# Performance work log

Measured on AMD Instinct MI355X. Metric: run time of the kernel, lower is better.

The kernel has to match this reference:

```python
import jax, jax.numpy as jnp
import numpy as np

B, L, E = 8, 2048, 128


def setup_inputs() -> dict:
    key = jax.random.key(0)
    k1, k2, k3, k4 = jax.random.split(key, 4)
    return {
        "Uq": jax.random.normal(k1, (B, L, E), dtype=jnp.float32),
        "Uid": jax.random.normal(k2, (B, L, E), dtype=jnp.float32),
        "mask": jnp.ones((L, L), dtype=jnp.float32),
        "Wc_w": jax.random.normal(k3, (3 * E,), dtype=jnp.float32) * 0.05,
        "Wc_b": jax.random.normal(k4, (), dtype=jnp.float32) * 0.05,
    }


def reference(Uq, Uid, mask, Wc_w, Wc_b):
    # Wc(cat(Uid, Uq, Uid*Uq)) decomposed into three direct projections —
    # exact same math as the Linear over the concatenation, never
    # materializing the [B, L, L, 3E] tensor.
    e = Uq.shape[-1]
    w_id, w_q, w_mul = Wc_w[:e], Wc_w[e:2 * e], Wc_w[2 * e:]
    s_id = jnp.einsum("bie,e->bi", Uid, w_id)          # [B, Lid]
    s_q = jnp.einsum("bje,e->bj", Uq, w_q)             # [B, Lq]
    s_mul = jnp.einsum("bie,bje,e->bij", Uid, Uq, w_mul)  # [B, Lid, Lq]
    S = (s_id[:, :, None] + s_q[:, None, :] + s_mul + Wc_b) * mask
    # S_D2Q = Softmax(dim=0) over the per-example [Lid, Lq] matrix -> axis=1
    P = jax.nn.softmax(S, axis=1)                      # [B, Lid, Lq]
    A_D2Q = jnp.einsum("bij,bje->bie", P, Uq)          # [B, Lid, E]
    M = jnp.einsum("bij,bkj->bik", P, P)               # P @ P^T, [B, Lid, Lid]
    A_Q2D = jnp.einsum("bik,bke->bie", M, Uid)         # [B, Lid, E]
    Vid = jnp.concatenate([Uid, A_D2Q, Uid * A_D2Q, Uid * A_Q2D], axis=-1)
    return Vid  # [B, Lid, 4E]
```

## Files before the change

### kernel.cpp

```cpp
#include <hip/hip_runtime.h>

#define L 2048
#define E 128
#define NB 8

typedef float f32x4 __attribute__((ext_vector_type(4)));
typedef short short8 __attribute__((ext_vector_type(8)));
typedef unsigned int u32;

static __device__ inline float bf2f(ushort u) {
  union { float f; u32 i; } v; v.i = ((u32)u) << 16; return v.f;
}
static __device__ inline ushort f2bf(float f) {
  union { float f; u32 i; } v; v.f = f;
  u32 x = v.i;
  return (ushort)((x + 0x7fffu + ((x >> 16) & 1u)) >> 16);
}

__device__ inline void glds16(const ushort* g, ushort* l) {
  __builtin_amdgcn_global_load_lds(
      (const __attribute__((address_space(1))) u32*)(const void*)g,
      (__attribute__((address_space(3))) u32*)(void*)l, 16, 0, 0);
}

__global__ __launch_bounds__(128) void k_prep(const float* __restrict__ Uq,
                                              const float* __restrict__ Uid,
                                              const float* __restrict__ Wcw,
                                              ushort* __restrict__ UqB,
                                              ushort* __restrict__ UidB,
                                              ushort* __restrict__ Uidw,
                                              float* __restrict__ s_id,
                                              float* __restrict__ s_q) {
  int r = blockIdx.x;
  int e = threadIdx.x;
  ushort uqu  = f2bf(Uq[(long)r * E + e]);
  ushort uidu = f2bf(Uid[(long)r * E + e]);
  float uqf = bf2f(uqu), uidf = bf2f(uidu);
  float wid  = bf2f(f2bf(Wcw[e]));
  float wq   = bf2f(f2bf(Wcw[E + e]));
  float wmul = bf2f(f2bf(Wcw[2 * E + e]));
  UqB[(long)r * E + e]  = uqu;
  UidB[(long)r * E + e] = uidu;
  Uidw[(long)r * E + e] = f2bf(uidf * wmul);
  float sid = uidf * wid, sq = uqf * wq;
  #pragma unroll
  for (int off = 32; off >= 1; off >>= 1) {
    sid += __shfl_down(sid, off, 64);
    sq  += __shfl_down(sq,  off, 64);
  }
  __shared__ float red[4];
  int wv = threadIdx.x >> 6;
  if ((threadIdx.x & 63) == 0) { red[wv * 2] = sid; red[wv * 2 + 1] = sq; }
  __syncthreads();
  if (threadIdx.x == 0) { s_id[r] = red[0] + red[2]; s_q[r] = red[1] + red[3]; }
}

__global__ __launch_bounds__(256) void k_maskT(const float* __restrict__ mask,
                                               ushort* __restrict__ maskT) {
  __shared__ ushort tile[32][33];
  int j0 = blockIdx.x * 32, i0 = blockIdx.y * 32;
  int tx = threadIdx.x, ty = threadIdx.y;
  #pragma unroll
  for (int r = ty; r < 32; r += 8)
    tile[r][tx] = f2bf(mask[(long)(i0 + r) * L + j0 + tx]);
  __syncthreads();
  #pragma unroll
  for (int r = ty; r < 32; r += 8)
    maskT[(long)(j0 + r) * L + i0 + tx] = tile[tx][r];
}

__global__ __launch_bounds__(256) void k_tr(const ushort* __restrict__ src,
                                            ushort* __restrict__ dst,
                                            int R, int C) {
  __shared__ ushort tile[32][33];
  long base = (long)blockIdx.z * R * C;
  src += base; dst += base;
  int c0 = blockIdx.x * 32, r0 = blockIdx.y * 32;
  int tx = threadIdx.x, ty = threadIdx.y;
  #pragma unroll
  for (int i = ty; i < 32; i += 8)
    tile[i][tx] = src[(long)(r0 + i) * C + c0 + tx];
  __syncthreads();
  #pragma unroll
  for (int i = ty; i < 32; i += 8)
    dst[(long)(c0 + i) * R + r0 + tx] = tile[tx][i];
}

__device__ inline void gemm128_loop(const ushort* __restrict__ A,
                                    const ushort* __restrict__ B,
                                    long ldA, long ldB, int K,
                                    f32x4 acc[4][4],
                                    ushort* ldsA, ushort* ldsB) {
  const int t = threadIdx.x;
  const int w = t >> 6, lane = t & 63;
  const int mrow = lane & 15, quad = lane >> 4;
  const int lr = lane >> 3;
  const int lc = ((lane & 7) ^ lr) * 8;
  const int mh = (w & 1) * 64, nh = (w >> 1) * 64;
  #pragma unroll
  for (int s = 0; s < 4; s++) {
    int row = w * 32 + s * 8 + lr;
    glds16(&A[(long)row * ldA + lc], &ldsA[w * 2048 + s * 512]);
    glds16(&B[(long)row * ldB + lc], &ldsB[w * 2048 + s * 512]);
  }
  __syncthreads();
  int cur = 0;
  for (int k0 = 0; k0 < K; k0 += 64) {
    int nxt = cur ^ 1;
    if (k0 + 64 < K) {
      #pragma unroll
      for (int s = 0; s < 4; s++) {
        int row = w * 32 + s * 8 + lr;
        glds16(&A[(long)row * ldA + k0 + 64 + lc], &ldsA[nxt * 8192 + w * 2048 + s * 512]);
        glds16(&B[(long)row * ldB + k0 + 64 + lc], &ldsB[nxt * 8192 + w * 2048 + s * 512]);
      }
    }
    const ushort* cA = &ldsA[cur * 8192];
    const ushort* cB = &ldsB[cur * 8192];
    #pragma unroll
    for (int kk = 0; kk < 2; kk++) {
      short8 av[4], bv[4];
      #pragma unroll
      for (int mi = 0; mi < 4; mi++)
        av[mi] = *(const short8*)&cA[(mh + mi * 16 + mrow) * 64 +
                                     ((kk * 32 + quad * 8) ^ ((mrow & 7) << 3))];
      #pragma unroll
      for (int ni = 0; ni < 4; ni++)
        bv[ni] = *(const short8*)&cB[(nh + ni * 16 + mrow) * 64 +
                                     ((kk * 32 + quad * 8) ^ ((mrow & 7) << 3))];
      #pragma unroll
      for (int mi = 0; mi < 4; mi++)
        #pragma unroll
        for (int ni = 0; ni < 4; ni++)
          acc[mi][ni] = __builtin_amdgcn_mfma_f32_16x16x32_bf16(av[mi], bv[ni], acc[mi][ni], 0, 0, 0);
    }
    __syncthreads();
    cur = nxt;
  }
}

__device__ inline void gemm64x128_loop(const ushort* __restrict__ A,
                                       const ushort* __restrict__ B,
                                       long ldA, long ldB, int K,
                                       f32x4 acc[2][4],
                                       ushort* ldsA, ushort* ldsB) {
  const int t = threadIdx.x;
  const int w = t >> 6, lane = t & 63;
  const int mrow = lane & 15, quad = lane >> 4;
  const int lr = lane >> 3;
  const int lc = ((lane & 7) ^ lr) * 8;
  const int mh = (w & 1) * 32, nh = (w >> 1) * 64;
  #pragma unroll
  for (int s = 0; s < 2; s++) {
    int row = w * 16 + s * 8 + lr;
    glds16(&A[(long)row * ldA + lc], &ldsA[w * 1024 + s * 512]);
  }
  #pragma unroll
  for (int s = 0; s < 4; s++) {
    int row = w * 32 + s * 8 + lr;
    glds16(&B[(long)row * ldB + lc], &ldsB[w * 2048 + s * 512]);
  }
  __syncthreads();
  int cur = 0;
  for (int k0 = 0; k0 < K; k0 += 64) {
    int nxt = cur ^ 1;
    if (k0 + 64 < K) {
      #pragma unroll
      for (int s = 0; s < 2; s++) {
        int row = w * 16 + s * 8 + lr;
        glds16(&A[(long)row * ldA + k0 + 64 + lc], &ldsA[nxt * 4096 + w * 1024 + s * 512]);
      }
      #pragma unroll
      for (int s = 0; s < 4; s++) {
        int row = w * 32 + s * 8 + lr;
        glds16(&B[(long)row * ldB + k0 + 64 + lc], &ldsB[nxt * 8192 + w * 2048 + s * 512]);
      }
    }
    const ushort* cA = &ldsA[cur * 4096];
    const ushort* cB = &ldsB[cur * 8192];
    #pragma unroll
    for (int kk = 0; kk < 2; kk++) {
      short8 av[2], bv[4];
      #pragma unroll
      for (int mi = 0; mi < 2; mi++)
        av[mi] = *(const short8*)&cA[(mh + mi * 16 + mrow) * 64 +
                                     ((kk * 32 + quad * 8) ^ ((mrow & 7) << 3))];
      #pragma unroll
      for (int ni = 0; ni < 4; ni++)
        bv[ni] = *(const short8*)&cB[(nh + ni * 16 + mrow) * 64 +
                                     ((kk * 32 + quad * 8) ^ ((mrow & 7) << 3))];
      #pragma unroll
      for (int mi = 0; mi < 2; mi++)
        #pragma unroll
        for (int ni = 0; ni < 4; ni++)
          acc[mi][ni] = __builtin_amdgcn_mfma_f32_16x16x32_bf16(av[mi], bv[ni], acc[mi][ni], 0, 0, 0);
    }
    __syncthreads();
    cur = nxt;
  }
}

__global__ __launch_bounds__(256) void k_scores(const ushort* __restrict__ Uq,
                                                const ushort* __restrict__ Uidw,
                                                const float* __restrict__ s_id,
                                                const float* __restrict__ s_q,
                                                const float* __restrict__ Wcb,
                                                const ushort* __restrict__ maskT,
                                                ushort* __restrict__ St,
                                                float* __restrict__ pm,
                                                float* __restrict__ ps, int b0) {
  __shared__ ushort lds[32768];
  ushort* ldsA = lds;
  ushort* ldsB = lds + 16384;
  int bz = blockIdx.z, b = b0 + bz;
  int m0 = blockIdx.x * 128;
  int n0 = blockIdx.y * 128;
  int tile_i = blockIdx.y;
  const ushort* A = Uq   + (long)b * L * E + (long)m0 * E;
  const ushort* B = Uidw + (long)b * L * E + (long)n0 * E;
  f32x4 acc[4][4] = {};
  gemm128_loop(A, B, E, E, E, acc, ldsA, ldsB);
  float bias = bf2f(f2bf(Wcb[0]));
  const int t = threadIdx.x, w = t >> 6, lane = t & 63;
  const int col = lane & 15, quad = lane >> 4;
  const int mh = (w & 1) * 64, nh = (w >> 1) * 64;

  __syncthreads();
  float sidv[4];
  #pragma unroll
  for (int ni = 0; ni < 4; ni++)
    sidv[ni] = s_id[b * L + n0 + nh + ni * 16 + col];
  #pragma unroll
  for (int mi = 0; mi < 4; mi++) {
    float sqv[4];
    #pragma unroll
    for (int rg = 0; rg < 4; rg++)
      sqv[rg] = s_q[b * L + m0 + mh + mi * 16 + quad * 4 + rg];
    #pragma unroll
    for (int ni = 0; ni < 4; ni++) {
      int cl = nh + ni * 16 + col;
      #pragma unroll
      for (int rg = 0; rg < 4; rg++) {
        int row = mh + mi * 16 + quad * 4 + rg;
        float v = acc[mi][ni][rg] + sqv[rg] + sidv[ni] + bias;
        lds[row * 128 + (cl ^ ((row & 7) << 3))] = f2bf(v);
      }
    }
  }
  __syncthreads();
  #pragma unroll
  for (int p = 0; p < 8; p++) {
    int r2 = p * 16 + (t >> 4);
    int cu = (t & 15) * 8;
    uint4 sv = *(const uint4*)&lds[r2 * 128 + (cu ^ ((r2 & 7) << 3))];
    int jg = m0 + r2;
    uint4 mv = *(const uint4*)&maskT[(long)jg * L + n0 + cu];
    ushort o[8]; float vv[8];
    const ushort* sp = (const ushort*)&sv;
    const ushort* mp = (const ushort*)&mv;
    #pragma unroll
    for (int k = 0; k < 8; k++) {
      o[k] = f2bf(bf2f(sp[k]) * bf2f(mp[k]));
      vv[k] = bf2f(o[k]);
    }
    *(uint4*)&St[(long)bz * L * L + (long)jg * L + n0 + cu] = *(const uint4*)&o[0];
    float lmx = vv[0];
    #pragma unroll
    for (int k = 1; k < 8; k++) lmx = fmaxf(lmx, vv[k]);
    #pragma unroll
    for (int off = 8; off >= 1; off >>= 1) lmx = fmaxf(lmx, __shfl_xor(lmx, off, 64));
    float lsum = 0.f;
    #pragma unroll
    for (int k = 0; k < 8; k++) lsum += __expf(vv[k] - lmx);
    #pragma unroll
    for (int off = 8; off >= 1; off >>= 1) lsum += __shfl_xor(lsum, off, 64);
    if ((t & 15) == 0) {
      long si = ((long)bz * L + jg) * 16 + tile_i;
      pm[si] = lmx; ps[si] = lsum;
    }
  }
}

__global__ __launch_bounds__(256) void k_redstats(const float* __restrict__ pm,
                                                  const float* __restrict__ ps,
                                                  float* __restrict__ mg,
                                                  float* __restrict__ lg) {
  int idx = blockIdx.x * 256 + threadIdx.x;
  const float* pmr = pm + (long)idx * 16;
  const float* psr = ps + (long)idx * 16;
  float m = pmr[0];
  #pragma unroll
  for (int k = 1; k < 16; k++) m = fmaxf(m, pmr[k]);
  float s = 0.f;
  #pragma unroll
  for (int k = 0; k < 16; k++) s += psr[k] * __expf(pmr[k] - m);
  mg[idx] = m;
  lg[idx] = 1.0f / s;
}

__global__ __launch_bounds__(256) void k_sm_apply(ushort* __restrict__ St,
                                                  ushort* __restrict__ P,
                                                  const float* __restrict__ mg,
                                                  const float* __restrict__ lg) {
  __shared__ ushort tl[4 * 1056];
  int bz = blockIdx.y;
  int t = threadIdx.x, wid = t >> 6, lane = t & 63;
  int flat = blockIdx.x * 4 + wid;
  int j0 = (flat >> 6) * 32;
  int i0 = (flat & 63) * 32;
  ushort* Sb = St + (long)bz * L * L;
  ushort* Pb = P  + (long)bz * L * L;
  ushort* wt = tl + wid * 1056;
  int r = lane >> 1, c0 = (lane & 1) * 16;
  float m   = mg[bz * L + j0 + r];
  float inv = lg[bz * L + j0 + r];
  ushort* src = Sb + (long)(j0 + r) * L + i0 + c0;
  uint4 q0 = *(const uint4*)src;
  uint4 q1 = *(const uint4*)(src + 8);
  ushort o[16];
  const ushort* pr = (const ushort*)&q0;
  #pragma unroll
  for (int k = 0; k < 8; k++) o[k] = f2bf(__expf(bf2f(pr[k]) - m) * inv);
  pr = (const ushort*)&q1;
  #pragma unroll
  for (int k = 0; k < 8; k++) o[8 + k] = f2bf(__expf(bf2f(pr[k]) - m) * inv);
  *(uint4*)src       = *(const uint4*)&o[0];
  *(uint4*)(src + 8) = *(const uint4*)&o[8];
  #pragma unroll
  for (int k = 0; k < 16; k++) tl[wid * 1056 + (c0 + k) * 33 + r] = o[k];
  asm volatile("s_waitcnt lgkmcnt(0)" ::: "memory");
  __builtin_amdgcn_sched_barrier(0);
  ushort po[16];
  #pragma unroll
  for (int k = 0; k < 16; k++) po[k] = wt[r * 33 + c0 + k];
  ushort* pd = Pb + (long)(i0 + r) * L + j0 + c0;
  *(uint4*)pd       = *(const uint4*)&po[0];
  *(uint4*)(pd + 8) = *(const uint4*)&po[8];
}

__global__ __launch_bounds__(256) void k_gemm_Tt(const ushort* __restrict__ UidT,
                                                 const ushort* __restrict__ Pt,
                                                 ushort* __restrict__ Tt, int b0) {
  __shared__ ushort lds[24576];
  ushort* ldsA = lds;
  ushort* ldsB = lds + 8192;
  int bz = blockIdx.z, b = b0 + bz;
  int e0 = (blockIdx.x & 1) * 64;
  int j0 = (blockIdx.x >> 1) * 128;
  const ushort* A = UidT + (long)b * E * L + (long)e0 * L;
  const ushort* B = Pt   + (long)bz * L * L + (long)j0 * L;
  f32x4 acc[2][4] = {};
  gemm64x128_loop(A, B, L, L, L, acc, ldsA, ldsB);
  const int t = threadIdx.x, w = t >> 6, lane = t & 63;
  const int col = lane & 15, quad = lane >> 4;
  const int mh = (w & 1) * 32, nh = (w >> 1) * 64;
  __syncthreads();
  #pragma unroll
  for (int mi = 0; mi < 2; mi++)
    #pragma unroll
    for (int ni = 0; ni < 4; ni++) {
      int cl = nh + ni * 16 + col;
      #pragma unroll
      for (int rg = 0; rg < 4; rg++) {
        int row = mh + mi * 16 + quad * 4 + rg;
        lds[row * 128 + (cl ^ ((row & 7) << 3))] = f2bf(acc[mi][ni][rg]);
      }
    }
  __syncthreads();
  #pragma unroll
  for (int p = 0; p < 4; p++) {
    int r2 = p * 16 + (t >> 4);
    int cu = (t & 15) * 8;
    uint4 v = *(const uint4*)&lds[r2 * 128 + (cu ^ ((r2 & 7) << 3))];
    *(uint4*)&Tt[(long)b * E * L + (long)(e0 + r2) * L + j0 + cu] = v;
  }
}

__global__ __launch_bounds__(256) void k_gemm_A(const ushort* __restrict__ P,
                                                const ushort* __restrict__ UqT,
                                                const ushort* __restrict__ Tt,
                                                const ushort* __restrict__ UidB,
                                                float* __restrict__ out, int b0) {
  __shared__ ushort ldsA[2 * 4096];
  __shared__ ushort ldsB[2 * 8192];
  int bz = blockIdx.z, b = b0 + bz;
  int m0 = blockIdx.x * 64;
  int n0 = blockIdx.y * 128;
  const ushort* A = P + (long)bz * L * L + (long)m0 * L;
  const ushort* B = (blockIdx.y == 0) ? (UqT + (long)b * E * L)
                                      : (Tt  + (long)b * E * L);
  f32x4 acc[2][4] = {};
  gemm64x128_loop(A, B, L, L, L, acc, ldsA, ldsB);
  const int t = threadIdx.x, w = t >> 6, lane = t & 63;
  const int col = lane & 15, quad = lane >> 4;
  const int mh = (w & 1) * 32, nh = (w >> 1) * 64;
  #pragma unroll
  for (int mi = 0; mi < 2; mi++)
    #pragma unroll
    for (int ni = 0; ni < 4; ni++)
      #pragma unroll
      for (int rg = 0; rg < 4; rg++) {
        int ig = m0 + mh + mi * 16 + quad * 4 + rg;
        int c  = n0 + nh + ni * 16 + col;
        float a = acc[mi][ni][rg];
        float uidf = bf2f(UidB[(long)b * L * E + (long)ig * E + (c & 127)]);
        long ob = ((long)b * L + ig) * 512;
        if (c < 128) {
          out[ob + c]       = uidf;
          out[ob + 128 + c] = a;
          out[ob + 256 + c] = uidf * a;
        } else {
          out[ob + 256 + c] = uidf * a;
        }
      }
}

extern "C" void kernel_launch(void* const* d_in, const int* in_sizes, int n_in,
                              void* d_out, int out_size, void* d_ws, size_t ws_size,
                              hipStream_t stream) {
  const float* Uq   = (const float*)d_in[0];
  const float* Uid  = (const float*)d_in[1];
  const float* mask = (const float*)d_in[2];
  const float* Wcw  = (const float*)d_in[3];
  const float* Wcb  = (const float*)d_in[4];
  float* out = (float*)d_out;

  char* ws = (char*)d_ws;
  size_t off = 0;
  auto alloc = [&](size_t bytes) -> void* {
    void* p = ws + off; off += (bytes + 255) & ~(size_t)255; return p;
  };
  const size_t nUb = (size_t)NB * L * E * 2;
  ushort* UqB   = (ushort*)alloc(nUb);
  ushort* UidB  = (ushort*)alloc(nUb);
  ushort* Uidw  = (ushort*)alloc(nUb);
  ushort* UqT   = (ushort*)alloc(nUb);
  ushort* UidT  = (ushort*)alloc(nUb);
  ushort* Tt    = (ushort*)alloc(nUb);
  ushort* maskT = (ushort*)alloc((size_t)L * L * 2);
  float*  s_id  = (float*)alloc((size_t)NB * L * 4);
  float*  s_q   = (float*)alloc((size_t)NB * L * 4);
  float*  mg    = (float*)alloc((size_t)NB * L * 4);
  float*  lg    = (float*)alloc((size_t)NB * L * 4);
  float*  pm    = (float*)alloc((size_t)NB * L * 16 * 4);
  float*  ps    = (float*)alloc((size_t)NB * L * 16 * 4);
  const size_t per_batch = (size_t)L * L * 2;
  size_t avail = (ws_size > off + 2 * per_batch) ? (ws_size - off) : 2 * per_batch;
  int nb_c = (int)(avail / (2 * per_batch));
  if (nb_c < 1) nb_c = 1;
  if (nb_c > NB) nb_c = NB;
  ushort* St = (ushort*)(ws + off);
  ushort* P  = (ushort*)(ws + off + nb_c * per_batch);

  dim3 tb(32, 8);
  k_prep<<<NB * L, E, 0, stream>>>(Uq, Uid, Wcw, UqB, UidB, Uidw, s_id, s_q);
  k_maskT<<<dim3(L / 32, L / 32), tb, 0, stream>>>(mask, maskT);
  k_tr<<<dim3(E / 32, L / 32, NB), tb, 0, stream>>>(UqB, UqT, L, E);
  k_tr<<<dim3(E / 32, L / 32, NB), tb, 0, stream>>>(UidB, UidT, L, E);

  for (int b0 = 0; b0 < NB; b0 += nb_c) {
    int nb = (NB - b0 < nb_c) ? (NB - b0) : nb_c;
    k_scores<<<dim3(L / 128, L / 128, nb), 256, 0, stream>>>(UqB, Uidw, s_id, s_q, Wcb, maskT, St, pm, ps, b0);
    k_redstats<<<dim3(nb * L / 256), 256, 0, stream>>>(pm, ps, mg, lg);
    k_sm_apply<<<dim3((L / 32) * (L / 32) / 4, nb), 256, 0, stream>>>(St, P, mg, lg);
    k_gemm_Tt<<<dim3(2 * (L / 128), 1, nb), 256, 0, stream>>>(UidT, St, Tt, b0);
    k_gemm_A<<<dim3(L / 64, 2, nb), 256, 0, stream>>>(P, UqT, Tt, UidB, out, b0);
  }
}
```

Baseline: 239.7 us.

## Single-buffer GEMM LDS, fold softmax stat reduction into apply, merge transposes

The GEMM inner loops drop LDS double-buffering and become load-sync-compute-sync per K step. This halves shared memory per block so more blocks can be resident, but global loads no longer overlap with MFMA work. The separate softmax statistics kernel is folded into k_sm_apply, where each block recomputes the per-row max and inverse sum for its 32 rows, and the two transpose launches are merged into one. Together these cut launches and intermediate buffers at the cost of some redundant statistic recomputation.

```diff
diff --git a/kernel.cpp b/kernel.cpp
--- a/kernel.cpp
+++ b/kernel.cpp
@@ -69,21 +69,24 @@
     maskT[(long)(j0 + r) * L + i0 + tx] = tile[tx][r];
 }
 
-__global__ __launch_bounds__(256) void k_tr(const ushort* __restrict__ src,
-                                            ushort* __restrict__ dst,
-                                            int R, int C) {
+__global__ __launch_bounds__(256) void k_tr2(const ushort* __restrict__ s1,
+                                             ushort* __restrict__ d1,
+                                             const ushort* __restrict__ s2,
+                                             ushort* __restrict__ d2) {
   __shared__ ushort tile[32][33];
-  long base = (long)blockIdx.z * R * C;
-  src += base; dst += base;
+  int zz = blockIdx.z;
+  long base = (long)(zz & (NB - 1)) * L * E;
+  const ushort* src = ((zz < NB) ? s1 : s2) + base;
+  ushort* dst = ((zz < NB) ? d1 : d2) + base;
   int c0 = blockIdx.x * 32, r0 = blockIdx.y * 32;
   int tx = threadIdx.x, ty = threadIdx.y;
   #pragma unroll
   for (int i = ty; i < 32; i += 8)
-    tile[i][tx] = src[(long)(r0 + i) * C + c0 + tx];
+    tile[i][tx] = src[(long)(r0 + i) * E + c0 + tx];
   __syncthreads();
   #pragma unroll
   for (int i = ty; i < 32; i += 8)
-    dst[(long)(c0 + i) * R + r0 + tx] = tile[tx][i];
+    dst[(long)(c0 + i) * L + r0 + tx] = tile[tx][i];
 }
 
 __device__ inline void gemm128_loop(const ushort* __restrict__ A,
@@ -97,45 +100,32 @@
   const int lr = lane >> 3;
   const int lc = ((lane & 7) ^ lr) * 8;
   const int mh = (w & 1) * 64, nh = (w >> 1) * 64;
-  #pragma unroll
-  for (int s = 0; s < 4; s++) {
-    int row = w * 32 + s * 8 + lr;
-    glds16(&A[(long)row * ldA + lc], &ldsA[w * 2048 + s * 512]);
-    glds16(&B[(long)row * ldB + lc], &ldsB[w * 2048 + s * 512]);
-  }
-  __syncthreads();
-  int cur = 0;
   for (int k0 = 0; k0 < K; k0 += 64) {
-    int nxt = cur ^ 1;
-    if (k0 + 64 < K) {
-      #pragma unroll
-      for (int s = 0; s < 4; s++) {
-        int row = w * 32 + s * 8 + lr;
-        glds16(&A[(long)row * ldA + k0 + 64 + lc], &ldsA[nxt * 8192 + w * 2048 + s * 512]);
-        glds16(&B[(long)row * ldB + k0 + 64 + lc], &ldsB[nxt * 8192 + w * 2048 + s * 512]);
-      }
-    }
-    const ushort* cA = &ldsA[cur * 8192];
-    const ushort* cB = &ldsB[cur * 8192];
+    __syncthreads();
+    #pragma unroll
+    for (int s = 0; s < 4; s++) {
+      int row = w * 32 + s * 8 + lr;
+      glds16(&A[(long)row * ldA + k0 + lc], &ldsA[w * 2048 + s * 512]);
+      glds16(&B[(long)row * ldB + k0 + lc], &ldsB[w * 2048 + s * 512]);
+    }
+    __syncthreads();
     #pragma unroll
     for (int kk = 0; kk < 2; kk++) {
       short8 av[4], bv[4];
       #pragma unroll
       for (int mi = 0; mi < 4; mi++)
-        av[mi] = *(const short8*)&cA[(mh + mi * 16 + mrow) * 64 +
-                                     ((kk * 32 + quad * 8) ^ ((mrow & 7) << 3))];
+        av[mi] = *(const short8*)&ldsA[(mh + mi * 16 + mrow) * 64 +
+                                       ((kk * 32 + quad * 8) ^ ((mrow & 7) << 3))];
       #pragma unroll
       for (int ni = 0; ni < 4; ni++)
-        bv[ni] = *(const short8*)&cB[(nh + ni * 16 + mrow) * 64 +
-                                     ((kk * 32 + quad * 8) ^ ((mrow & 7) << 3))];
+        bv[ni] = *(const short8*)&ldsB[(nh + ni * 16 + mrow) * 64 +
+                                       ((kk * 32 + quad * 8) ^ ((mrow & 7) << 3))];
       #pragma unroll
       for (int mi = 0; mi < 4; mi++)
         #pragma unroll
         for (int ni = 0; ni < 4; ni++)
           acc[mi][ni] = __builtin_amdgcn_mfma_f32_16x16x32_bf16(av[mi], bv[ni], acc[mi][ni], 0, 0, 0);
     }
-    __syncthreads();
-    cur = nxt;
   }
 }
 
@@ -150,53 +140,36 @@
   const int lr = lane >> 3;
   const int lc = ((lane & 7) ^ lr) * 8;
   const int mh = (w & 1) * 32, nh = (w >> 1) * 64;
-  #pragma unroll
-  for (int s = 0; s < 2; s++) {
-    int row = w * 16 + s * 8 + lr;
-    glds16(&A[(long)row * ldA + lc], &ldsA[w * 1024 + s * 512]);
-  }
-  #pragma unroll
-  for (int s = 0; s < 4; s++) {
-    int row = w * 32 + s * 8 + lr;
-    glds16(&B[(long)row * ldB + lc], &ldsB[w * 2048 + s * 512]);
-  }
-  __syncthreads();
-  int cur = 0;
   for (int k0 = 0; k0 < K; k0 += 64) {
-    int nxt = cur ^ 1;
-    if (k0 + 64 < K) {
-      #pragma unroll
-      for (int s = 0; s < 2; s++) {
-        int row = w * 16 + s * 8 + lr;
-        glds16(&A[(long)row * ldA + k0 + 64 + lc], &ldsA[nxt * 4096 + w * 1024 + s * 512]);
-      }
-      #pragma unroll
-      for (int s = 0; s < 4; s++) {
-        int row = w * 32 + s * 8 + lr;
-        glds16(&B[(long)row * ldB + k0 + 64 + lc], &ldsB[nxt * 8192 + w * 2048 + s * 512]);
-      }
-    }
-    const ushort* cA = &ldsA[cur * 4096];
-    const ushort* cB = &ldsB[cur * 8192];
+    __syncthreads();
+    #pragma unroll
+    for (int s = 0; s < 2; s++) {
+      int row = w * 16 + s * 8 + lr;
+      glds16(&A[(long)row * ldA + k0 + lc], &ldsA[w * 1024 + s * 512]);
+    }
+    #pragma unroll
+    for (int s = 0; s < 4; s++) {
+      int row = w * 32 + s * 8 + lr;
+      glds16(&B[(long)row * ldB + k0 + lc], &ldsB[w * 2048 + s * 512]);
+    }
+    __syncthreads();
     #pragma unroll
     for (int kk = 0; kk < 2; kk++) {
       short8 av[2], bv[4];
       #pragma unroll
       for (int mi = 0; mi < 2; mi++)
-        av[mi] = *(const short8*)&cA[(mh + mi * 16 + mrow) * 64 +
-                                     ((kk * 32 + quad * 8) ^ ((mrow & 7) << 3))];
+        av[mi] = *(const short8*)&ldsA[(mh + mi * 16 + mrow) * 64 +
+                                       ((kk * 32 + quad * 8) ^ ((mrow & 7) << 3))];
       #pragma unroll
       for (int ni = 0; ni < 4; ni++)
-        bv[ni] = *(const short8*)&cB[(nh + ni * 16 + mrow) * 64 +
-                                     ((kk * 32 + quad * 8) ^ ((mrow & 7) << 3))];
+        bv[ni] = *(const short8*)&ldsB[(nh + ni * 16 + mrow) * 64 +
+                                       ((kk * 32 + quad * 8) ^ ((mrow & 7) << 3))];
       #pragma unroll
       for (int mi = 0; mi < 2; mi++)
         #pragma unroll
         for (int ni = 0; ni < 4; ni++)
           acc[mi][ni] = __builtin_amdgcn_mfma_f32_16x16x32_bf16(av[mi], bv[ni], acc[mi][ni], 0, 0, 0);
     }
-    __syncthreads();
-    cur = nxt;
   }
 }
 
@@ -209,9 +182,9 @@
                                                 ushort* __restrict__ St,
                                                 float* __restrict__ pm,
                                                 float* __restrict__ ps, int b0) {
-  __shared__ ushort lds[32768];
+  __shared__ ushort lds[16384];
   ushort* ldsA = lds;
-  ushort* ldsB = lds + 16384;
+  ushort* ldsB = lds + 8192;
   int bz = blockIdx.z, b = b0 + bz;
   int m0 = blockIdx.x * 128;
   int n0 = blockIdx.y * 128;
@@ -281,39 +254,35 @@
   }
 }
 
-__global__ __launch_bounds__(256) void k_redstats(const float* __restrict__ pm,
-                                                  const float* __restrict__ ps,
-                                                  float* __restrict__ mg,
-                                                  float* __restrict__ lg) {
-  int idx = blockIdx.x * 256 + threadIdx.x;
-  const float* pmr = pm + (long)idx * 16;
-  const float* psr = ps + (long)idx * 16;
-  float m = pmr[0];
-  #pragma unroll
-  for (int k = 1; k < 16; k++) m = fmaxf(m, pmr[k]);
-  float s = 0.f;
-  #pragma unroll
-  for (int k = 0; k < 16; k++) s += psr[k] * __expf(pmr[k] - m);
-  mg[idx] = m;
-  lg[idx] = 1.0f / s;
-}
-
 __global__ __launch_bounds__(256) void k_sm_apply(ushort* __restrict__ St,
                                                   ushort* __restrict__ P,
-                                                  const float* __restrict__ mg,
-                                                  const float* __restrict__ lg) {
+                                                  const float* __restrict__ pm,
+                                                  const float* __restrict__ ps) {
   __shared__ ushort tl[4 * 1056];
+  __shared__ float smM[32], smI[32];
   int bz = blockIdx.y;
   int t = threadIdx.x, wid = t >> 6, lane = t & 63;
   int flat = blockIdx.x * 4 + wid;
   int j0 = (flat >> 6) * 32;
   int i0 = (flat & 63) * 32;
+  if (t < 32) {
+    const float* pmr = pm + ((long)bz * L + j0 + t) * 16;
+    const float* psr = ps + ((long)bz * L + j0 + t) * 16;
+    float m = pmr[0];
+    #pragma unroll
+    for (int k = 1; k < 16; k++) m = fmaxf(m, pmr[k]);
+    float s = 0.f;
+    #pragma unroll
+    for (int k = 0; k < 16; k++) s += psr[k] * __expf(pmr[k] - m);
+    smM[t] = m; smI[t] = 1.0f / s;
+  }
+  __syncthreads();
   ushort* Sb = St + (long)bz * L * L;
   ushort* Pb = P  + (long)bz * L * L;
   ushort* wt = tl + wid * 1056;
   int r = lane >> 1, c0 = (lane & 1) * 16;
-  float m   = mg[bz * L + j0 + r];
-  float inv = lg[bz * L + j0 + r];
+  float m   = smM[r];
+  float inv = smI[r];
   ushort* src = Sb + (long)(j0 + r) * L + i0 + c0;
   uint4 q0 = *(const uint4*)src;
   uint4 q1 = *(const uint4*)(src + 8);
@@ -327,7 +296,7 @@
   *(uint4*)src       = *(const uint4*)&o[0];
   *(uint4*)(src + 8) = *(const uint4*)&o[8];
   #pragma unroll
-  for (int k = 0; k < 16; k++) tl[wid * 1056 + (c0 + k) * 33 + r] = o[k];
+  for (int k = 0; k < 16; k++) wt[(c0 + k) * 33 + r] = o[k];
   asm volatile("s_waitcnt lgkmcnt(0)" ::: "memory");
   __builtin_amdgcn_sched_barrier(0);
   ushort po[16];
@@ -341,9 +310,9 @@
 __global__ __launch_bounds__(256) void k_gemm_Tt(const ushort* __restrict__ UidT,
                                                  const ushort* __restrict__ Pt,
                                                  ushort* __restrict__ Tt, int b0) {
-  __shared__ ushort lds[24576];
+  __shared__ ushort lds[12288];
   ushort* ldsA = lds;
-  ushort* ldsB = lds + 8192;
+  ushort* ldsB = lds + 4096;
   int bz = blockIdx.z, b = b0 + bz;
   int e0 = (blockIdx.x & 1) * 64;
   int j0 = (blockIdx.x >> 1) * 128;
@@ -381,8 +350,8 @@
                                                 const ushort* __restrict__ Tt,
                                                 const ushort* __restrict__ UidB,
                                                 float* __restrict__ out, int b0) {
-  __shared__ ushort ldsA[2 * 4096];
-  __shared__ ushort ldsB[2 * 8192];
+  __shared__ ushort ldsA[64 * 64];
+  __shared__ ushort ldsB[128 * 64];
   int bz = blockIdx.z, b = b0 + bz;
   int m0 = blockIdx.x * 64;
   int n0 = blockIdx.y * 128;
@@ -440,8 +409,6 @@
   ushort* maskT = (ushort*)alloc((size_t)L * L * 2);
   float*  s_id  = (float*)alloc((size_t)NB * L * 4);
   float*  s_q   = (float*)alloc((size_t)NB * L * 4);
-  float*  mg    = (float*)alloc((size_t)NB * L * 4);
-  float*  lg    = (float*)alloc((size_t)NB * L * 4);
   float*  pm    = (float*)alloc((size_t)NB * L * 16 * 4);
   float*  ps    = (float*)alloc((size_t)NB * L * 16 * 4);
   const size_t per_batch = (size_t)L * L * 2;
@@ -455,14 +422,12 @@
   dim3 tb(32, 8);
   k_prep<<<NB * L, E, 0, stream>>>(Uq, Uid, Wcw, UqB, UidB, Uidw, s_id, s_q);
   k_maskT<<<dim3(L / 32, L / 32), tb, 0, stream>>>(mask, maskT);
-  k_tr<<<dim3(E / 32, L / 32, NB), tb, 0, stream>>>(UqB, UqT, L, E);
-  k_tr<<<dim3(E / 32, L / 32, NB), tb, 0, stream>>>(UidB, UidT, L, E);
+  k_tr2<<<dim3(E / 32, L / 32, 2 * NB), tb, 0, stream>>>(UqB, UqT, UidB, UidT);
 
   for (int b0 = 0; b0 < NB; b0 += nb_c) {
     int nb = (NB - b0 < nb_c) ? (NB - b0) : nb_c;
     k_scores<<<dim3(L / 128, L / 128, nb), 256, 0, stream>>>(UqB, Uidw, s_id, s_q, Wcb, maskT, St, pm, ps, b0);
-    k_redstats<<<dim3(nb * L / 256), 256, 0, stream>>>(pm, ps, mg, lg);
-    k_sm_apply<<<dim3((L / 32) * (L / 32) / 4, nb), 256, 0, stream>>>(St, P, mg, lg);
+    k_sm_apply<<<dim3((L / 32) * (L / 32) / 4, nb), 256, 0, stream>>>(St, P, pm, ps);
     k_gemm_Tt<<<dim3(2 * (L / 128), 1, nb), 256, 0, stream>>>(UidT, St, Tt, b0);
     k_gemm_A<<<dim3(L / 64, 2, nb), 256, 0, stream>>>(P, UqT, Tt, UidB, out, b0);
   }
```

Measured after the change: 233.9 us. -2.4%, faster.
